# Performance work log

Hardware: AMD Instinct MI355X
Metric: run time of the kernel (lower is better)

The kernel has to match this reference:

```python
import jax, jax.numpy as jnp
import numpy as np

POOLER_SIZE = 56
SPATIAL_SCALE = 0.25
B, P, K, H, W, A = 4, 512, 4, 200, 336, 14
IMG_H, IMG_W = H / SPATIAL_SCALE, W / SPATIAL_SCALE


def _roi_align_one(feat, boxes):
    """torchvision RoIAlign (aligned=False, sampling_ratio=1).
    feat: [K, H, W]; boxes: [P, 4] as (x1, y1, x2, y2) in image coords.
    Returns [P, K, ps, ps]."""
    Kc, Hf, Wf = feat.shape
    ps = POOLER_SIZE
    s = SPATIAL_SCALE
    x1 = boxes[:, 0] * s
    y1 = boxes[:, 1] * s
    x2 = boxes[:, 2] * s
    y2 = boxes[:, 3] * s
    rw = jnp.maximum(x2 - x1, 1.0)  # non-aligned mode clamps roi size to >= 1
    rh = jnp.maximum(y2 - y1, 1.0)
    bw = rw / ps
    bh = rh / ps
    grid = jnp.arange(ps, dtype=feat.dtype) + 0.5  # sampling_ratio=1 -> bin center
    xs = x1[:, None] + grid[None, :] * bw[:, None]  # [P, ps]
    ys = y1[:, None] + grid[None, :] * bh[:, None]  # [P, ps]
    xx = jnp.broadcast_to(xs[:, None, :], (xs.shape[0], ps, ps))  # [P, ps, ps]
    yy = jnp.broadcast_to(ys[:, :, None], (ys.shape[0], ps, ps))
    valid = (yy > -1.0) & (yy < Hf) & (xx > -1.0) & (xx < Wf)
    y = jnp.clip(yy, 0.0, Hf - 1)
    x = jnp.clip(xx, 0.0, Wf - 1)
    y0 = jnp.floor(y).astype(jnp.int32)
    x0 = jnp.floor(x).astype(jnp.int32)
    y1i = jnp.minimum(y0 + 1, Hf - 1)
    x1i = jnp.minimum(x0 + 1, Wf - 1)
    ly = y - y0
    lx = x - x0
    f = feat.reshape(Kc, Hf * Wf)

    def gather(yi, xi):
        idx = (yi * Wf + xi).reshape(-1)
        return jnp.take(f, idx, axis=1).reshape((Kc,) + yi.shape)  # [K, P, ps, ps]

    w00 = ((1.0 - ly) * (1.0 - lx))[None]
    w01 = ((1.0 - ly) * lx)[None]
    w10 = (ly * (1.0 - lx))[None]
    w11 = (ly * lx)[None]
    v = (gather(y0, x0) * w00 + gather(y0, x1i) * w01 +
         gather(y1i, x0) * w10 + gather(y1i, x1i) * w11)
    v = v * valid[None].astype(feat.dtype)
    return jnp.transpose(v, (1, 0, 2, 3))  # [P, K, ps, ps]


def _bilinear_resize_ac(x, ps):
    """F.interpolate(mode='bilinear', align_corners=True) on last two dims (square a->ps)."""
    a = x.shape[-1]
    src = jnp.arange(ps, dtype=x.dtype) * ((a - 1) / (ps - 1))
    i0 = jnp.clip(jnp.floor(src).astype(jnp.int32), 0, a - 2)
    i1 = i0 + 1
    t = src - i0.astype(x.dtype)
    rows = x[..., i0, :] * (1.0 - t)[:, None] + x[..., i1, :] * t[:, None]  # [..., ps, a]
    out = rows[..., :, i0] * (1.0 - t) + rows[..., :, i1] * t  # [..., ps, ps]
    return out


def setup_inputs() -> dict:
    key = jax.random.key(0)
    k1, k2, k3, k4, k5, k6 = jax.random.split(key, 6)
    bases = jax.random.normal(k1, (B, K, H, W), dtype=jnp.float32)
    attention_proposals = jax.random.normal(k2, (B, P, K, A, A), dtype=jnp.float32)
    # realistic boxes inside an 800x1344 image
    x1 = jax.random.uniform(k3, (B, P)) * (IMG_W - 64.0)
    y1 = jax.random.uniform(k4, (B, P)) * (IMG_H - 64.0)
    bw = 32.0 + jax.random.uniform(k5, (B, P)) * 256.0
    bh = 32.0 + jax.random.uniform(k6, (B, P)) * 256.0
    x2 = jnp.minimum(x1 + bw, IMG_W)
    y2 = jnp.minimum(y1 + bh, IMG_H)
    box_proposals = jnp.stack([x1, y1, x2, y2], axis=-1).astype(jnp.float32)  # [B, P, 4]
    return {"bases": bases, "box_proposals": box_proposals,
            "attention_proposals": attention_proposals}


def reference(bases, box_proposals, attention_proposals):
    ps = POOLER_SIZE
    rois = jax.vmap(_roi_align_one)(bases, box_proposals)  # [B, P, K, ps, ps]
    attn = _bilinear_resize_ac(attention_proposals, ps)    # [B, P, K, ps, ps]
    attn = jax.nn.softmax(attn, axis=2)                    # softmax over num_bases
    return (attn * rois).sum(axis=2)                       # [B, P, ps, ps]
```

## Files before the change

kernel.cpp:

```cpp
#include <hip/hip_runtime.h>
#include <math.h>

#define B_  4
#define P_  512
#define K_  4
#define H_  200
#define W_  336
#define A_  14
#define PS_ 56
#define SCALE_ 0.25f
#define HW_   (H_ * W_)
#define PLB_  (HW_ * 16)
#define ROWB_ (W_ * 16)
#define RROWB_ (PS_ * K_ * 4)

#if __has_builtin(__builtin_amdgcn_exp2f)
#define EXP2F(x) __builtin_amdgcn_exp2f(x)
#else
#define EXP2F(x) exp2f(x)
#endif

__global__ __launch_bounds__(256) void transpose_bases(
    const float* __restrict__ bases, float4* __restrict__ ws)
{
    const int i = blockIdx.x * 256 + threadIdx.x;
    if (i >= B_ * HW_) return;
    const int b = i / HW_;
    const int r = i - b * HW_;
    const float* src = bases + (size_t)b * (K_ * HW_) + r;
    float4 v;
    v.x = src[0 * HW_];
    v.y = src[1 * HW_];
    v.z = src[2 * HW_];
    v.w = src[3 * HW_];
    ws[i] = v;
}

__global__ __launch_bounds__(448) void blender_kernel(
    const float4* __restrict__ wsb,
    const float* __restrict__ boxes,
    const float* __restrict__ attn,
    float* __restrict__ out)
{
    const int tid = threadIdx.x;
    const int bp  = blockIdx.x;
    const int b   = bp >> 9;

    __shared__ float  smTile[K_ * A_ * A_];
    __shared__ float  smR[A_ * PS_ * K_];
    __shared__ float4 smX[PS_];
    __shared__ float4 smY[PS_];
    __shared__ float2 smAY[PS_];

    const float* ap = attn + (size_t)bp * (K_ * A_ * A_);
    for (int i = tid; i < K_ * A_ * A_; i += 448)
        smTile[i] = __builtin_nontemporal_load(ap + i);

    const float* bx = boxes + (size_t)bp * 4;
    const float rr = 13.0f / 55.0f;

    if (tid < PS_) {
        const int px = tid;
        const float x1 = bx[0] * SCALE_;
        const float x2 = bx[2] * SCALE_;
        const float bw = fmaxf(x2 - x1, 1.0f) * (1.0f / PS_);
        const float sx = x1 + (px + 0.5f) * bw;
        const float vx = (sx > -1.0f && sx < (float)W_) ? 1.0f : 0.0f;
        const float cx = fminf(fmaxf(sx, 0.0f), (float)(W_ - 1));
        const int   x0 = (int)cx;
        const float lx = cx - (float)x0;
        float4 v;
        if (x0 >= W_ - 1) {
            v.x = __int_as_float((W_ - 2) * 16);
            v.y = 0.0f;
            v.z = vx;
        } else {
            v.x = __int_as_float(x0 * 16);
            v.y = (1.0f - lx) * vx;
            v.z = lx * vx;
        }
        v.w = 0.0f;
        smX[px] = v;
    } else if (tid >= 64 && tid < 64 + PS_) {
        const int py = tid - 64;
        const float y1 = bx[1] * SCALE_;
        const float y2 = bx[3] * SCALE_;
        const float bh = fmaxf(y2 - y1, 1.0f) * (1.0f / PS_);
        const float sy = y1 + (py + 0.5f) * bh;
        const float vy = (sy > -1.0f && sy < (float)H_) ? 1.0f : 0.0f;
        const float cy = fminf(fmaxf(sy, 0.0f), (float)(H_ - 1));
        const int   y0 = (int)cy;
        const int   y1i = min(y0 + 1, H_ - 1);
        const float ly = cy - (float)y0;
        float4 v;
        v.x = __int_as_float(y0 * ROWB_);
        v.y = __int_as_float((y1i - y0) * ROWB_);
        v.z = (1.0f - ly) * vy;
        v.w = ly * vy;
        smY[py] = v;
        const float srcy = (float)py * rr;
        const int iy0 = min((int)srcy, A_ - 2);
        float2 a;
        a.x = __int_as_float(iy0 * RROWB_);
        a.y = srcy - (float)iy0;
        smAY[py] = a;
    }
    __syncthreads();

    const float LOG2E = 1.4426950408889634f;
    for (int i = tid; i < K_ * A_ * PS_; i += 448) {
        const int k  = i / (A_ * PS_);
        const int r1 = i - k * (A_ * PS_);
        const int ay = r1 / PS_;
        const int px = r1 - ay * PS_;
        const float srcx = (float)px * rr;
        const int ix0 = min((int)srcx, A_ - 2);
        const float tx = srcx - (float)ix0;
        const float* t = smTile + k * (A_ * A_) + ay * A_ + ix0;
        smR[(ay * PS_ + px) * K_ + k] = (t[0] + tx * (t[1] - t[0])) * LOG2E;
    }
    __syncthreads();

    const char* fb = (const char*)wsb + (size_t)b * PLB_;
    float* outp = out + (size_t)bp * (PS_ * PS_);

    const int px  = tid % PS_;
    const int py0 = tid / PS_;

    const float4 X = smX[px];
    const unsigned xb = (unsigned)__float_as_int(X.x);
    const float wl = X.y, wh = X.z;
    const char* smRbase = (const char*)smR + (px << 4);

    #pragma unroll
    for (int t = 0; t < 7; ++t) {
        const int py = py0 + 8 * t;
        const float4 Y  = smY[py];
        const float2 AY = smAY[py];
        const unsigned o0 = (unsigned)__float_as_int(Y.x) + xb;
        const unsigned o1 = o0 + (unsigned)__float_as_int(Y.y);
        const float wy0 = Y.z, wy1 = Y.w;
        const float ty  = AY.y;

        const float4 q00 = *(const float4*)(fb + o0);
        const float4 q01 = *(const float4*)(fb + o0 + 16);
        const float4 q10 = *(const float4*)(fb + o1);
        const float4 q11 = *(const float4*)(fb + o1 + 16);

        float vx0, vx1, vx2, vx3;
        {
            const float r0x = fmaf(q01.x, wh, q00.x * wl);
            const float r0y = fmaf(q01.y, wh, q00.y * wl);
            const float r0z = fmaf(q01.z, wh, q00.z * wl);
            const float r0w = fmaf(q01.w, wh, q00.w * wl);
            const float r1x = fmaf(q11.x, wh, q10.x * wl);
            const float r1y = fmaf(q11.y, wh, q10.y * wl);
            const float r1z = fmaf(q11.z, wh, q10.z * wl);
            const float r1w = fmaf(q11.w, wh, q10.w * wl);
            vx0 = fmaf(r1x, wy1, r0x * wy0);
            vx1 = fmaf(r1y, wy1, r0y * wy0);
            vx2 = fmaf(r1z, wy1, r0z * wy0);
            vx3 = fmaf(r1w, wy1, r0w * wy0);
        }

        const float4 a0v = *(const float4*)(smRbase + __float_as_int(AY.x));
        const float4 a1v = *(const float4*)(smRbase + __float_as_int(AY.x) + RROWB_);

        const float e0 = EXP2F(fmaf(ty, a1v.x - a0v.x, a0v.x));
        const float e1 = EXP2F(fmaf(ty, a1v.y - a0v.y, a0v.y));
        const float e2 = EXP2F(fmaf(ty, a1v.z - a0v.z, a0v.z));
        const float e3 = EXP2F(fmaf(ty, a1v.w - a0v.w, a0v.w));

        const float s   = (e0 + e1) + (e2 + e3);
        float acc = e0 * vx0;
        acc = fmaf(e1, vx1, acc);
        acc = fmaf(e2, vx2, acc);
        acc = fmaf(e3, vx3, acc);

        __builtin_nontemporal_store(acc * __builtin_amdgcn_rcpf(s),
                                    outp + tid + 448 * t);
    }
}

extern "C" void kernel_launch(void* const* d_in, const int* in_sizes, int n_in,
                              void* d_out, int out_size, void* d_ws, size_t ws_size,
                              hipStream_t stream) {
    const float* bases = (const float*)d_in[0];
    const float* boxes = (const float*)d_in[1];
    const float* attn  = (const float*)d_in[2];
    float* out = (float*)d_out;
    float4* wsb = (float4*)d_ws;

    transpose_bases<<<dim3((B_ * HW_ + 255) / 256), dim3(256), 0, stream>>>(bases, wsb);
    blender_kernel<<<dim3(B_ * P_), dim3(448), 0, stream>>>(wsb, boxes, attn, out);
}
```

Baseline: 91.10 us.

## Pack bases as bf16 with right-neighbour pixel and software-pipeline gathers

The transpose kernel now stores each pixel's four channels plus its right neighbour's four channels as bf16 in one 16-byte word. Each bilinear sample then needs two 16-byte loads instead of four. The main loop is restructured to issue the next row's loads before computing the current one, so gather latency overlaps with compute. The cost is reduced precision (bf16 feature values), which may exceed the output tolerance. It also adds extra reads in the transpose kernel, and the x-edge handling moves into the packed layout.

```diff
diff --git a/kernel.cpp b/kernel.cpp
--- a/kernel.cpp
+++ b/kernel.cpp
@@ -9,9 +9,9 @@
 #define A_  14
 #define PS_ 56
 #define SCALE_ 0.25f
-#define HW_   (H_ * W_)
-#define PLB_  (HW_ * 16)
-#define ROWB_ (W_ * 16)
+#define HW_    (H_ * W_)
+#define PLB_   (HW_ * 16)
+#define ROWB_  (W_ * 16)
 #define RROWB_ (PS_ * K_ * 4)
 
 #if __has_builtin(__builtin_amdgcn_exp2f)
@@ -20,24 +20,38 @@
 #define EXP2F(x) exp2f(x)
 #endif
 
+static __device__ __forceinline__ unsigned f2bf(float x) {
+    unsigned u = __float_as_uint(x);
+    return (u + 0x7fffu + ((u >> 16) & 1u)) >> 16;
+}
+static __device__ __forceinline__ unsigned pk2(float a, float b) {
+    return f2bf(a) | (f2bf(b) << 16);
+}
+#define LOF(u) __uint_as_float((u) << 16)
+#define HIF(u) __uint_as_float((u) & 0xffff0000u)
+
 __global__ __launch_bounds__(256) void transpose_bases(
-    const float* __restrict__ bases, float4* __restrict__ ws)
+    const float* __restrict__ bases, uint4* __restrict__ ws)
 {
     const int i = blockIdx.x * 256 + threadIdx.x;
     if (i >= B_ * HW_) return;
     const int b = i / HW_;
     const int r = i - b * HW_;
+    const int x = r % W_;
+    const int dn = (x < W_ - 1) ? 1 : 0;
     const float* src = bases + (size_t)b * (K_ * HW_) + r;
-    float4 v;
-    v.x = src[0 * HW_];
-    v.y = src[1 * HW_];
-    v.z = src[2 * HW_];
-    v.w = src[3 * HW_];
-    ws[i] = v;
+    const float v0 = src[0 * HW_],      v1 = src[1 * HW_];
+    const float v2 = src[2 * HW_],      v3 = src[3 * HW_];
+    const float n0 = src[0 * HW_ + dn], n1 = src[1 * HW_ + dn];
+    const float n2 = src[2 * HW_ + dn], n3 = src[3 * HW_ + dn];
+    uint4 w;
+    w.x = pk2(v0, v1); w.y = pk2(v2, v3);
+    w.z = pk2(n0, n1); w.w = pk2(n2, n3);
+    ws[i] = w;
 }
 
 __global__ __launch_bounds__(448) void blender_kernel(
-    const float4* __restrict__ wsb,
+    const uint4* __restrict__ wsb,
     const float* __restrict__ boxes,
     const float* __restrict__ attn,
     float* __restrict__ out)
@@ -70,15 +84,9 @@
         const int   x0 = (int)cx;
         const float lx = cx - (float)x0;
         float4 v;
-        if (x0 >= W_ - 1) {
-            v.x = __int_as_float((W_ - 2) * 16);
-            v.y = 0.0f;
-            v.z = vx;
-        } else {
-            v.x = __int_as_float(x0 * 16);
-            v.y = (1.0f - lx) * vx;
-            v.z = lx * vx;
-        }
+        v.x = __int_as_float(x0 * 16);
+        v.y = (1.0f - lx) * vx;
+        v.z = lx * vx;
         v.w = 0.0f;
         smX[px] = v;
     } else if (tid >= 64 && tid < 64 + PS_) {
@@ -132,54 +140,64 @@
     const float wl = X.y, wh = X.z;
     const char* smRbase = (const char*)smR + (px << 4);
 
-    #pragma unroll
-    for (int t = 0; t < 7; ++t) {
+    struct PState {
+        uint4 r0, r1;
+        float wy0, wy1, ty;
+        int   ayo;
+    };
+
+    auto issue = [&](int t, PState& S) {
         const int py = py0 + 8 * t;
         const float4 Y  = smY[py];
         const float2 AY = smAY[py];
         const unsigned o0 = (unsigned)__float_as_int(Y.x) + xb;
         const unsigned o1 = o0 + (unsigned)__float_as_int(Y.y);
-        const float wy0 = Y.z, wy1 = Y.w;
-        const float ty  = AY.y;
-
-        const float4 q00 = *(const float4*)(fb + o0);
-        const float4 q01 = *(const float4*)(fb + o0 + 16);
-        const float4 q10 = *(const float4*)(fb + o1);
-        const float4 q11 = *(const float4*)(fb + o1 + 16);
-
-        float vx0, vx1, vx2, vx3;
-        {
-            const float r0x = fmaf(q01.x, wh, q00.x * wl);
-            const float r0y = fmaf(q01.y, wh, q00.y * wl);
-            const float r0z = fmaf(q01.z, wh, q00.z * wl);
-            const float r0w = fmaf(q01.w, wh, q00.w * wl);
-            const float r1x = fmaf(q11.x, wh, q10.x * wl);
-            const float r1y = fmaf(q11.y, wh, q10.y * wl);
-            const float r1z = fmaf(q11.z, wh, q10.z * wl);
-            const float r1w = fmaf(q11.w, wh, q10.w * wl);
-            vx0 = fmaf(r1x, wy1, r0x * wy0);
-            vx1 = fmaf(r1y, wy1, r0y * wy0);
-            vx2 = fmaf(r1z, wy1, r0z * wy0);
-            vx3 = fmaf(r1w, wy1, r0w * wy0);
-        }
-
-        const float4 a0v = *(const float4*)(smRbase + __float_as_int(AY.x));
-        const float4 a1v = *(const float4*)(smRbase + __float_as_int(AY.x) + RROWB_);
-
+        S.r0 = *(const uint4*)(fb + o0);
+        S.r1 = *(const uint4*)(fb + o1);
+        S.wy0 = Y.z; S.wy1 = Y.w;
+        S.ty = AY.y; S.ayo = __float_as_int(AY.x);
+    };
+
+    auto compute = [&](const PState& S) -> float {
+        const float wy0 = S.wy0, wy1 = S.wy1, ty = S.ty;
+        const float r0a = fmaf(LOF(S.r0.z), wh, LOF(S.r0.x) * wl);
+        const float r0b = fmaf(HIF(S.r0.z), wh, HIF(S.r0.x) * wl);
+        const float r0c = fmaf(LOF(S.r0.w), wh, LOF(S.r0.y) * wl);
+        const float r0d = fmaf(HIF(S.r0.w), wh, HIF(S.r0.y) * wl);
+        const float r1a = fmaf(LOF(S.r1.z), wh, LOF(S.r1.x) * wl);
+        const float r1b = fmaf(HIF(S.r1.z), wh, HIF(S.r1.x) * wl);
+        const float r1c = fmaf(LOF(S.r1.w), wh, LOF(S.r1.y) * wl);
+        const float r1d = fmaf(HIF(S.r1.w), wh, HIF(S.r1.y) * wl);
+        const float v0 = fmaf(r1a, wy1, r0a * wy0);
+        const float v1 = fmaf(r1b, wy1, r0b * wy0);
+        const float v2 = fmaf(r1c, wy1, r0c * wy0);
+        const float v3 = fmaf(r1d, wy1, r0d * wy0);
+
+        const float4 a0v = *(const float4*)(smRbase + S.ayo);
+        const float4 a1v = *(const float4*)(smRbase + S.ayo + RROWB_);
         const float e0 = EXP2F(fmaf(ty, a1v.x - a0v.x, a0v.x));
         const float e1 = EXP2F(fmaf(ty, a1v.y - a0v.y, a0v.y));
         const float e2 = EXP2F(fmaf(ty, a1v.z - a0v.z, a0v.z));
         const float e3 = EXP2F(fmaf(ty, a1v.w - a0v.w, a0v.w));
 
-        const float s   = (e0 + e1) + (e2 + e3);
-        float acc = e0 * vx0;
-        acc = fmaf(e1, vx1, acc);
-        acc = fmaf(e2, vx2, acc);
-        acc = fmaf(e3, vx3, acc);
-
-        __builtin_nontemporal_store(acc * __builtin_amdgcn_rcpf(s),
-                                    outp + tid + 448 * t);
+        const float s = (e0 + e1) + (e2 + e3);
+        float acc = e0 * v0;
+        acc = fmaf(e1, v1, acc);
+        acc = fmaf(e2, v2, acc);
+        acc = fmaf(e3, v3, acc);
+        return acc * __builtin_amdgcn_rcpf(s);
+    };
+
+    PState SA, SB;
+    issue(0, SA);
+    #pragma unroll
+    for (int g = 0; g < 6; g += 2) {
+        issue(g + 1, SB);
+        __builtin_nontemporal_store(compute(SA), outp + tid + 448 * g);
+        issue(g + 2, SA);
+        __builtin_nontemporal_store(compute(SB), outp + tid + 448 * (g + 1));
     }
+    __builtin_nontemporal_store(compute(SA), outp + tid + 448 * 6);
 }
 
 extern "C" void kernel_launch(void* const* d_in, const int* in_sizes, int n_in,
@@ -189,7 +207,7 @@
     const float* boxes = (const float*)d_in[1];
     const float* attn  = (const float*)d_in[2];
     float* out = (float*)d_out;
-    float4* wsb = (float4*)d_ws;
+    uint4* wsb = (uint4*)d_ws;
 
     transpose_bases<<<dim3((B_ * HW_ + 255) / 256), dim3(256), 0, stream>>>(bases, wsb);
     blender_kernel<<<dim3(B_ * P_), dim3(448), 0, stream>>>(wsb, boxes, attn, out);
```

Result: no change. 90.29 us (-0.9%).
